# Performance work log

Measured on AMD Instinct MI355X. Metric: run time of the kernel, lower is better.

## Reference

```python
import jax, jax.numpy as jnp
import numpy as np

D_MODEL = 1024
D_INNER = 2048   # expand * d_model
D_STATE = 128
NGROUPS = 1
HEADDIM = 64
NHEADS = D_INNER // HEADDIM  # 32
D_CONV = 4
CHUNK = 256
EPS = 1e-5


def setup_inputs() -> dict:
    key = jax.random.key(0)
    ks = jax.random.split(key, 6)
    B, L = 2, 2048
    d_in_proj = 2 * D_INNER + 2 * NGROUPS * D_STATE + NHEADS  # 4384
    conv_dim = D_INNER + 2 * NGROUPS * D_STATE                # 2304
    u = jax.random.normal(ks[0], (B, L, D_MODEL), jnp.float32)
    W_in = jax.random.normal(ks[1], (d_in_proj, D_MODEL), jnp.float32) * 0.02
    conv_w = jax.random.normal(ks[2], (conv_dim, D_CONV), jnp.float32) * 0.2
    conv_b = jnp.zeros((conv_dim,), jnp.float32)
    # dt_bias = inverse-softplus of dt ~ LogUniform(1e-3, 1e-1), as in __init__
    dt = jnp.exp(jax.random.uniform(ks[3], (NHEADS,), jnp.float32)
                 * (np.log(0.1) - np.log(0.001)) + np.log(0.001))
    dt_bias = dt + jnp.log(-jnp.expm1(-dt))
    A_log = jnp.log(jax.random.uniform(ks[4], (NHEADS,), jnp.float32,
                                       minval=1.0, maxval=16.0))
    D_param = jnp.ones((NHEADS,), jnp.float32)
    norm_w = jnp.ones((D_INNER,), jnp.float32)
    return dict(u=u, W_in=W_in, conv_w=conv_w, conv_b=conv_b,
                dt_bias=dt_bias, A_log=A_log, D_param=D_param, norm_w=norm_w)


def _segsum(x):
    # x: (..., T) -> (..., T, T); entry [i, s] = sum_{j in (s, i]} x_j, -inf above diag
    T = x.shape[-1]
    csum = jnp.cumsum(x, -1)
    diff = csum[..., :, None] - csum[..., None, :]
    mask = jnp.tril(jnp.ones((T, T), dtype=bool))
    return jnp.where(mask, diff, -jnp.inf)


def reference(u, W_in, conv_w, conv_b, dt_bias, A_log, D_param, norm_w):
    B, L, _ = u.shape
    zxbcdt = u @ W_in.T  # (B, L, 2*d_inner + 2*g*N + H)
    z, xBC, dt = jnp.split(zxbcdt, [D_INNER, 2 * D_INNER + 2 * NGROUPS * D_STATE], axis=-1)

    # fused causal depthwise conv1d + silu
    xp = jnp.pad(xBC, ((0, 0), (D_CONV - 1, 0), (0, 0)))
    xc = conv_b
    for k in range(D_CONV):
        xc = xc + xp[:, k:k + L, :] * conv_w[:, k]
    xBC = jax.nn.silu(xc)

    x, Bm, Cm = jnp.split(xBC, [D_INNER, D_INNER + NGROUPS * D_STATE], axis=-1)
    dt = jax.nn.softplus(dt + dt_bias)          # (B, L, H)
    A = -jnp.exp(A_log)                          # (H,)

    x = x.reshape(B, L, NHEADS, HEADDIM)
    Bh = jnp.repeat(Bm.reshape(B, L, NGROUPS, D_STATE), NHEADS // NGROUPS, axis=2)
    Ch = jnp.repeat(Cm.reshape(B, L, NGROUPS, D_STATE), NHEADS // NGROUPS, axis=2)

    # chunked SSD (Mamba2) scan
    nc = L // CHUNK
    xc_ = x.reshape(B, nc, CHUNK, NHEADS, HEADDIM)
    dtc = dt.reshape(B, nc, CHUNK, NHEADS)
    Bc = Bh.reshape(B, nc, CHUNK, NHEADS, D_STATE)
    Cc = Ch.reshape(B, nc, CHUNK, NHEADS, D_STATE)

    a = jnp.moveaxis(dtc * A, -1, 2)             # (B, nc, H, cs)
    a_cum = jnp.cumsum(a, -1)
    Lmat = jnp.exp(_segsum(a))                   # (B, nc, H, cs, cs), lower-tri decay
    xdt = xc_ * dtc[..., None]                   # (B, nc, cs, H, P)

    # intra-chunk (diagonal blocks)
    Y_diag = jnp.einsum('bclhn,bcshn,bchls,bcshp->bclhp', Cc, Bc, Lmat, xdt)

    # chunk-final states and inter-chunk recurrence
    decay_states = jnp.exp(a_cum[..., -1:] - a_cum)         # (B, nc, H, cs)
    states = jnp.einsum('bclhn,bchl,bclhp->bchpn', Bc, decay_states, xdt)
    chunk_decay = jnp.exp(a_cum[..., -1])                   # (B, nc, H)

    def scan_fn(carry, inp):
        s, d = inp                                           # (B,H,P,N), (B,H)
        return carry * d[..., None, None] + s, carry

    init = jnp.zeros((B, NHEADS, HEADDIM, D_STATE), xdt.dtype)
    _, prev_states = jax.lax.scan(scan_fn, init,
                                  (jnp.moveaxis(states, 1, 0),
                                   jnp.moveaxis(chunk_decay, 1, 0)))
    prev_states = jnp.moveaxis(prev_states, 0, 1)            # (B, nc, H, P, N)

    Y_off = jnp.einsum('bclhn,bchpn,bchl->bclhp', Cc, prev_states, jnp.exp(a_cum))

    Y = (Y_diag + Y_off).reshape(B, L, NHEADS, HEADDIM) + D_param[None, None, :, None] * x
    y = Y.reshape(B, L, D_INNER)

    # gated RMSNorm (norm_before_gate=False: gate first, then normalize)
    g = y * jax.nn.silu(z)
    g = g * jax.lax.rsqrt(jnp.mean(g * g, axis=-1, keepdims=True) + EPS) * norm_w
    return g
```

## Files before the change

### kernel.cpp

```cpp
#include <hip/hip_runtime.h>
#include <cstdint>
#include <cmath>

#define KDIM    1024
#define DPROJ   4384
#define NPAD    4480
#define CONVDIM 2304
#define SEQ     2048
#define BATCH   2
#define MROWS   4096
#define NHEADS  32
#define HEADDIM 64
#define DSTATE  128
#define CHUNK   256
#define NCHUNK  8
#define DINNER  2048
#define EPS     1e-5f

typedef unsigned short u16;
typedef float  f32x4  __attribute__((ext_vector_type(4)));
typedef __bf16 bf16x8 __attribute__((ext_vector_type(8)));
typedef u16    u16x8  __attribute__((ext_vector_type(8)));

__device__ __forceinline__ u16 f2bf(float f){
  unsigned u = __builtin_bit_cast(unsigned, f);
  u += 0x7fffu + ((u >> 16) & 1u);
  return (u16)(u >> 16);
}
__device__ __forceinline__ float bf2f(u16 s){
  unsigned u = ((unsigned)s) << 16;
  return __builtin_bit_cast(float, u);
}
__device__ __forceinline__ void gl_lds16(const void* g, void* l){
  __builtin_amdgcn_global_load_lds((const __attribute__((address_space(1))) void*)g,
                                   (__attribute__((address_space(3))) void*)l, 16, 0, 0);
}
__device__ __forceinline__ float sigmoidf_(float x){ return 1.f / (1.f + expf(-x)); }

__global__ __launch_bounds__(256) void k_cvt(const float* __restrict__ u_in, u16* __restrict__ u_out,
                                             const float* __restrict__ w_in, u16* __restrict__ w_out){
  int bid = blockIdx.x;
  const float* in; u16* out; size_t i; int wpath = 0;
  if(bid < 4096){ in = u_in; out = u_out; i = ((size_t)bid * 256 + threadIdx.x) * 4; }
  else          { in = w_in; out = w_out; i = ((size_t)(bid - 4096) * 256 + threadIdx.x) * 4; wpath = 1; }
  float4 v = make_float4(0.f,0.f,0.f,0.f);
  if(!wpath || (int)(i >> 10) < DPROJ) v = *(const float4*)(in + i);
  unsigned a = (unsigned)f2bf(v.x) | ((unsigned)f2bf(v.y) << 16);
  unsigned b = (unsigned)f2bf(v.z) | ((unsigned)f2bf(v.w) << 16);
  uint2 o; o.x = a; o.y = b;
  *(uint2*)(out + i) = o;
}

__global__ __launch_bounds__(256) void k_gemm(const u16* __restrict__ A, const u16* __restrict__ B,
                                              u16* __restrict__ zq, float* __restrict__ dtraw){
  __shared__ u16 As[128*32];
  __shared__ u16 Bs[128*32];
  int tid = threadIdx.x;
  int gid = blockIdx.x;
  int mG  = gid / (35*8);
  int rem = gid % (35*8);
  int nblk = rem / 8;
  int mblk = mG*8 + (rem & 7);
  int m0 = mblk * 128, n0 = nblk * 128;
  int w = tid >> 6, lane = tid & 63, r = lane & 15, q = lane >> 4;
  int wm = (w >> 1) * 64, wn = (w & 1) * 64;
  f32x4 acc[4][4] = {};
  const u16* Ag0 = A + (size_t)(m0 +       (tid >> 2)) * KDIM + (tid & 3) * 8;
  const u16* Ag1 = A + (size_t)(m0 + 64 +  (tid >> 2)) * KDIM + (tid & 3) * 8;
  const u16* Bg0 = B + (size_t)(n0 +       (tid >> 2)) * KDIM + (tid & 3) * 8;
  const u16* Bg1 = B + (size_t)(n0 + 64 +  (tid >> 2)) * KDIM + (tid & 3) * 8;
  for(int kt = 0; kt < KDIM/32; kt++){
    int k0 = kt * 32;
    gl_lds16(Ag0 + k0, &As[(size_t)tid * 8]);
    gl_lds16(Ag1 + k0, &As[((size_t)tid + 256) * 8]);
    gl_lds16(Bg0 + k0, &Bs[(size_t)tid * 8]);
    gl_lds16(Bg1 + k0, &Bs[((size_t)tid + 256) * 8]);
    __syncthreads();
    bf16x8 af[4], bfm[4];
    #pragma unroll
    for(int i = 0; i < 4; i++) af[i]  = *(const bf16x8*)&As[(wm + i*16 + r) * 32 + q*8];
    #pragma unroll
    for(int j = 0; j < 4; j++) bfm[j] = *(const bf16x8*)&Bs[(wn + j*16 + r) * 32 + q*8];
    #pragma unroll
    for(int i = 0; i < 4; i++)
      #pragma unroll
      for(int j = 0; j < 4; j++)
        acc[i][j] = __builtin_amdgcn_mfma_f32_16x16x32_bf16(af[i], bfm[j], acc[i][j], 0, 0, 0);
    __syncthreads();
  }
  #pragma unroll
  for(int i = 0; i < 4; i++)
    #pragma unroll
    for(int j = 0; j < 4; j++)
      #pragma unroll
      for(int e = 0; e < 4; e++){
        int row = m0 + wm + i*16 + q*4 + e;
        int col = n0 + wn + j*16 + r;
        zq[(size_t)row * NPAD + col] = f2bf(acc[i][j][e]);
        if(nblk == 34) dtraw[(size_t)row * 128 + (col - 4352)] = acc[i][j][e];
      }
}

__global__ __launch_bounds__(256) void k_conv(const u16* __restrict__ zq,
                                              const float* __restrict__ cw,
                                              const float* __restrict__ cb,
                                              u16* __restrict__ xq, u16* __restrict__ xqT,
                                              u16* __restrict__ Bq, u16* __restrict__ Cq){
  int c0 = blockIdx.x * 64;
  int l0 = blockIdx.y * 64;
  int b  = blockIdx.z;
  int lane = threadIdx.x & 63;
  int c = c0 + lane;
  int lb = l0 + (threadIdx.x >> 6) * 16;
  float wt0 = cw[c*4+0], wt1 = cw[c*4+1], wt2 = cw[c*4+2], wt3 = cw[c*4+3];
  float bias = cb[c];
  const u16* zrow = zq + (size_t)(b*SEQ) * NPAD + 2048 + c;
  float w0 = (lb-3 >= 0) ? bf2f(zrow[(size_t)(lb-3)*NPAD]) : 0.f;
  float w1 = (lb-2 >= 0) ? bf2f(zrow[(size_t)(lb-2)*NPAD]) : 0.f;
  float w2 = (lb-1 >= 0) ? bf2f(zrow[(size_t)(lb-1)*NPAD]) : 0.f;
  u16 vals[16];
  #pragma unroll
  for(int rr = 0; rr < 16; rr++){
    float in3 = bf2f(zrow[(size_t)(lb+rr)*NPAD]);
    float a = bias + w0*wt0 + w1*wt1 + w2*wt2 + in3*wt3;
    vals[rr] = f2bf(a * sigmoidf_(a));
    w0 = w1; w1 = w2; w2 = in3;
  }
  if(blockIdx.x < 32){
    #pragma unroll
    for(int rr = 0; rr < 16; rr++)
      xq[(size_t)(b*SEQ + lb + rr) * DINNER + c] = vals[rr];
    int h = c0 >> 6;
    u16* dst = xqT + ((size_t)((b*32 + h)*64) + lane) * SEQ + lb;
    u16x8 v0, v1;
    #pragma unroll
    for(int m = 0; m < 8; m++){ v0[m] = vals[m]; v1[m] = vals[8+m]; }
    *(u16x8*)dst = v0;
    *(u16x8*)(dst + 8) = v1;
  } else {
    u16* dst; int col;
    if(blockIdx.x < 34){ dst = Bq; col = c0 - 2048 + lane; }
    else               { dst = Cq; col = c0 - 2176 + lane; }
    #pragma unroll
    for(int rr = 0; rr < 16; rr++)
      dst[(size_t)(b*SEQ + lb + rr) * 128 + col] = vals[rr];
  }
}

__global__ __launch_bounds__(256) void k_acum(const float* __restrict__ dtraw,
                                              const float* __restrict__ dt_bias,
                                              const float* __restrict__ A_log,
                                              float* __restrict__ dtb,
                                              float* __restrict__ acum,
                                              float* __restrict__ cdec){
  int bid = blockIdx.x;
  int h = bid & 31, c = (bid >> 5) & 7, b = bid >> 8;
  int t = threadIdx.x;
  __shared__ float sb[256];
  size_t row = (size_t)(b*SEQ + c*CHUNK + t);
  float v = dtraw[row * 128 + h] + dt_bias[h];
  float dt = (v > 20.f) ? v : log1pf(expf(v));
  dtb[row * 32 + h] = dt;
  float Ah = -expf(A_log[h]);
  float a = dt * Ah;
  sb[t] = a; __syncthreads();
  for(int off = 1; off < 256; off <<= 1){
    float vv = (t >= off) ? sb[t - off] : 0.f;
    __syncthreads();
    sb[t] += vv;
    __syncthreads();
  }
  float ac = sb[t];
  acum[(size_t)bid * 256 + t] = ac;
  if(t == 255) cdec[bid] = expf(ac);
}

__global__ __launch_bounds__(256) void k_states(const u16* __restrict__ xqT, const u16* __restrict__ Bq,
                                                const float* __restrict__ dtb,
                                                const float* __restrict__ acum,
                                                float* __restrict__ states){
  int bid = blockIdx.x;
  int h = bid & 31, c = (bid >> 5) & 7, b = bid >> 8;
  int tid = threadIdx.x;
  int w = tid >> 6, lane = tid & 63, r = lane & 15, q = lane >> 4;
  __shared__ u16 bT[128*72];
  size_t rowB = (size_t)(b*SEQ + c*CHUNK);
  const u16* xrow = xqT + (size_t)((b*32 + h)*64) * SEQ + c*CHUNK;
  float alast = acum[(size_t)bid * 256 + 255];
  f32x4 acc[4][2] = {};
  for(int slab = 0; slab < 4; slab++){
    int lb = slab * 64;
    int l = lane;
    float f = expf(alast - acum[(size_t)bid * 256 + lb + l]) * dtb[(rowB + lb + l) * 32 + h];
    __syncthreads();
    const u16* bp = Bq + (rowB + lb + l) * 128 + w*32;
    #pragma unroll
    for(int k = 0; k < 4; k++){
      u16x8 v = *(const u16x8*)(bp + k*8);
      #pragma unroll
      for(int m = 0; m < 8; m++)
        bT[(w*32 + k*8 + m)*72 + l] = f2bf(bf2f(v[m]) * f);
    }
    __syncthreads();
    #pragma unroll
    for(int ks = 0; ks < 2; ks++){
      bf16x8 af[4], bfr[2];
      #pragma unroll
      for(int i = 0; i < 4; i++)
        af[i] = *(const bf16x8*)&xrow[(size_t)(i*16 + r) * SEQ + lb + ks*32 + q*8];
      #pragma unroll
      for(int j = 0; j < 2; j++) bfr[j] = *(const bf16x8*)&bT[(w*32 + j*16 + r)*72 + ks*32 + q*8];
      #pragma unroll
      for(int i = 0; i < 4; i++)
        #pragma unroll
        for(int j = 0; j < 2; j++)
          acc[i][j] = __builtin_amdgcn_mfma_f32_16x16x32_bf16(af[i], bfr[j], acc[i][j], 0, 0, 0);
    }
  }
  #pragma unroll
  for(int i = 0; i < 4; i++)
    #pragma unroll
    for(int j = 0; j < 2; j++)
      #pragma unroll
      for(int e = 0; e < 4; e++){
        int p = i*16 + q*4 + e;
        int n = w*32 + j*16 + r;
        states[((size_t)bid * 64 + p) * 128 + n] = acc[i][j][e];
      }
}

__global__ __launch_bounds__(256) void k_scan(const float* __restrict__ states,
                                              const float* __restrict__ cdec,
                                              u16* __restrict__ prevb){
  size_t i = (size_t)blockIdx.x * 256 + threadIdx.x;
  int n = (int)(i & 127), p = (int)((i >> 7) & 63), h = (int)((i >> 13) & 31), b = (int)(i >> 18);
  float carry = 0.f;
  for(int c = 0; c < NCHUNK; c++){
    int bch = (b*8 + c)*32 + h;
    size_t off = ((size_t)bch * 64 + p) * 128 + n;
    float s = states[off];
    prevb[off] = f2bf(carry);
    carry = carry * cdec[bch] + s;
  }
}

__global__ __launch_bounds__(128) void k_y(const u16* __restrict__ xqT, const u16* __restrict__ Bq,
                                           const u16* __restrict__ Cq, const float* __restrict__ dtb,
                                           const float* __restrict__ acum, const u16* __restrict__ prevb,
                                           u16* __restrict__ yq){
  int bid = blockIdx.x;
  int bch = bid >> 1, pr = bid & 1;
  int h = bch & 31, c = (bch >> 5) & 7, b = bch >> 8;
  int tid = threadIdx.x;
  int w2 = tid >> 6, lane = tid & 63, r = lane & 15, q = lane >> 4;
  int lt = pr ? (1 + w2) : (w2 * 3);
  int l0 = lt * 64;
  __shared__ float acl[256];
  __shared__ float dts[256];
  __shared__ u16 G[2][64*72];
  size_t rowC = (size_t)(b*SEQ + c*CHUNK);
  #pragma unroll
  for(int it = 0; it < 2; it++){
    int s = it*128 + tid;
    acl[s] = acum[(size_t)bch * 256 + s];
    dts[s] = dtb[(rowC + s) * 32 + h];
  }
  __syncthreads();
  bf16x8 cf[4][4];
  #pragma unroll
  for(int i = 0; i < 4; i++)
    #pragma unroll
    for(int ks = 0; ks < 4; ks++)
      cf[i][ks] = *(const bf16x8*)&Cq[(rowC + l0 + i*16 + r) * 128 + ks*32 + q*8];
  f32x4 accY[4][4] = {};
  #pragma unroll
  for(int ks = 0; ks < 4; ks++){
    #pragma unroll
    for(int j = 0; j < 4; j++){
      bf16x8 bfr = *(const bf16x8*)&prevb[((size_t)bch * 64 + j*16 + r) * 128 + ks*32 + q*8];
      #pragma unroll
      for(int i = 0; i < 4; i++)
        accY[i][j] = __builtin_amdgcn_mfma_f32_16x16x32_bf16(cf[i][ks], bfr, accY[i][j], 0, 0, 0);
    }
  }
  #pragma unroll
  for(int i = 0; i < 4; i++)
    #pragma unroll
    for(int e = 0; e < 4; e++){
      float sc = expf(acl[l0 + i*16 + q*4 + e]);
      #pragma unroll
      for(int j = 0; j < 4; j++) accY[i][j][e] *= sc;
    }
  const u16* xrow = xqT + (size_t)((b*32 + h)*64) * SEQ + c*CHUNK;
  u16* Gw = G[w2];
  for(int st = 0; st <= lt; st++){
    int s0 = st * 64;
    f32x4 accS[4][4] = {};
    #pragma unroll
    for(int ks = 0; ks < 4; ks++){
      #pragma unroll
      for(int j = 0; j < 4; j++){
        bf16x8 bfr = *(const bf16x8*)&Bq[(rowC + s0 + j*16 + r) * 128 + ks*32 + q*8];
        #pragma unroll
        for(int i = 0; i < 4; i++)
          accS[i][j] = __builtin_amdgcn_mfma_f32_16x16x32_bf16(cf[i][ks], bfr, accS[i][j], 0, 0, 0);
      }
    }
    #pragma unroll
    for(int i = 0; i < 4; i++)
      #pragma unroll
      for(int j = 0; j < 4; j++)
        #pragma unroll
        for(int e = 0; e < 4; e++){
          int ll = l0 + i*16 + q*4 + e;
          int ss = s0 + j*16 + r;
          float v = (ll >= ss) ? accS[i][j][e] * expf(acl[ll] - acl[ss]) * dts[ss] : 0.f;
          Gw[(i*16 + q*4 + e)*72 + j*16 + r] = f2bf(v);
        }
    #pragma unroll
    for(int ks = 0; ks < 2; ks++){
      bf16x8 gf[4], xf[4];
      #pragma unroll
      for(int i = 0; i < 4; i++) gf[i] = *(const bf16x8*)&Gw[(i*16 + r)*72 + ks*32 + q*8];
      #pragma unroll
      for(int j = 0; j < 4; j++)
        xf[j] = *(const bf16x8*)&xrow[(size_t)(j*16 + r) * SEQ + s0 + ks*32 + q*8];
      #pragma unroll
      for(int i = 0; i < 4; i++)
        #pragma unroll
        for(int j = 0; j < 4; j++)
          accY[i][j] = __builtin_amdgcn_mfma_f32_16x16x32_bf16(gf[i], xf[j], accY[i][j], 0, 0, 0);
    }
  }
  #pragma unroll
  for(int i = 0; i < 4; i++)
    #pragma unroll
    for(int j = 0; j < 4; j++)
      #pragma unroll
      for(int e = 0; e < 4; e++){
        int ll = l0 + i*16 + q*4 + e;
        int p = j*16 + r;
        yq[(rowC + ll) * (size_t)DINNER + h*64 + p] = f2bf(accY[i][j][e]);
      }
}

__global__ __launch_bounds__(256) void k_norm(const u16* __restrict__ yq, const u16* __restrict__ xq,
                                              const u16* __restrict__ zq, const float* __restrict__ Dp,
                                              const float* __restrict__ nw, float* __restrict__ out){
  int bl = blockIdx.x;
  int t = threadIdx.x;
  float Dh = Dp[t >> 3];
  u16x8 yv = *(const u16x8*)(yq + (size_t)bl * DINNER + t*8);
  u16x8 xv = *(const u16x8*)(xq + (size_t)bl * DINNER + t*8);
  u16x8 zv = *(const u16x8*)(zq + (size_t)bl * NPAD + t*8);
  float g[8];
  float ss = 0.f;
  #pragma unroll
  for(int m = 0; m < 8; m++){
    float y = bf2f(yv[m]) + Dh * bf2f(xv[m]);
    float z = bf2f(zv[m]);
    float v = y * (z * sigmoidf_(z));
    g[m] = v;
    ss += v * v;
  }
  #pragma unroll
  for(int off = 32; off > 0; off >>= 1) ss += __shfl_down(ss, off, 64);
  __shared__ float wsum[4];
  if((t & 63) == 0) wsum[t >> 6] = ss;
  __syncthreads();
  float tot = wsum[0] + wsum[1] + wsum[2] + wsum[3];
  float scale = rsqrtf(tot / (float)DINNER + EPS);
  float4 o0, o1;
  o0.x = g[0]*scale*nw[t*8+0]; o0.y = g[1]*scale*nw[t*8+1];
  o0.z = g[2]*scale*nw[t*8+2]; o0.w = g[3]*scale*nw[t*8+3];
  o1.x = g[4]*scale*nw[t*8+4]; o1.y = g[5]*scale*nw[t*8+5];
  o1.z = g[6]*scale*nw[t*8+6]; o1.w = g[7]*scale*nw[t*8+7];
  *(float4*)(out + (size_t)bl * DINNER + t*8)     = o0;
  *(float4*)(out + (size_t)bl * DINNER + t*8 + 4) = o1;
}

extern "C" void kernel_launch(void* const* d_in, const int* in_sizes, int n_in,
                              void* d_out, int out_size, void* d_ws, size_t ws_size,
                              hipStream_t stream){
  const float* u    = (const float*)d_in[0];
  const float* W    = (const float*)d_in[1];
  const float* cw   = (const float*)d_in[2];
  const float* cb   = (const float*)d_in[3];
  const float* dtbi = (const float*)d_in[4];
  const float* Alog = (const float*)d_in[5];
  const float* Dp   = (const float*)d_in[6];
  const float* nw   = (const float*)d_in[7];
  float* out = (float*)d_out;

  char* ws = (char*)d_ws;
  size_t off = 0;
  auto alloc = [&](size_t bytes) -> void* {
    void* p = ws + off;
    off += (bytes + 255) & ~(size_t)255;
    return p;
  };
  u16*   u_bf    = (u16*)  alloc((size_t)MROWS * KDIM * 2);
  u16*   W_bf    = (u16*)  alloc((size_t)NPAD * KDIM * 2);
  u16*   zq      = (u16*)  alloc((size_t)MROWS * NPAD * 2);
  float* dtraw   = (float*)alloc((size_t)MROWS * 128 * 4);
  u16*   xq      = (u16*)  alloc((size_t)MROWS * DINNER * 2);
  u16*   xqT     = (u16*)  alloc((size_t)MROWS * DINNER * 2);
  u16*   Bq      = (u16*)  alloc((size_t)MROWS * 128 * 2);
  u16*   Cq      = (u16*)  alloc((size_t)MROWS * 128 * 2);
  float* dtb     = (float*)alloc((size_t)MROWS * 32 * 4);
  float* acum    = (float*)alloc((size_t)512 * 256 * 4);
  float* cdec    = (float*)alloc((size_t)512 * 4);
  float* states  = (float*)alloc((size_t)512 * 64 * 128 * 4);
  u16*   prevb   = (u16*)  alloc((size_t)512 * 64 * 128 * 2);
  u16*   yq      = (u16*)  alloc((size_t)MROWS * DINNER * 2);

  k_cvt<<<4096 + 4480, 256, 0, stream>>>(u, u_bf, W, W_bf);
  k_gemm<<<35*32, 256, 0, stream>>>(u_bf, W_bf, zq, dtraw);
  k_conv<<<dim3(36, 32, 2), 256, 0, stream>>>(zq, cw, cb, xq, xqT, Bq, Cq);
  k_acum<<<512, 256, 0, stream>>>(dtraw, dtbi, Alog, dtb, acum, cdec);
  k_states<<<512, 256, 0, stream>>>(xqT, Bq, dtb, acum, states);
  k_scan<<<((size_t)BATCH*NHEADS*64*128)/256, 256, 0, stream>>>(states, cdec, prevb);
  k_y<<<1024, 128, 0, stream>>>(xqT, Bq, Cq, dtb, acum, prevb, yq);
  k_norm<<<MROWS, 256, 0, stream>>>(yq, xq, zq, Dp, nw, out);
}
```

Baseline: 305.3 us.

## Deepen GEMM K-tile, vectorize conv over four channels, store states in bf16

The input-projection GEMM now stages 64-wide K tiles in LDS instead of 32, halving the number of barrier-separated iterations and issuing more MFMAs per sync. The conv kernel has each thread handle four adjacent channels, using 8-byte vector loads and stores and a quarter as many blocks. The chunk states buffer is stored as bf16 rather than fp32, halving the traffic between the states and scan kernels at some cost in precision of the inter-chunk recurrence input.

Result: no change. 304.1 us (-0.4%).

```diff
diff --git a/kernel.cpp b/kernel.cpp
--- a/kernel.cpp
+++ b/kernel.cpp
@@ -21,6 +21,7 @@
 typedef float  f32x4  __attribute__((ext_vector_type(4)));
 typedef __bf16 bf16x8 __attribute__((ext_vector_type(8)));
 typedef u16    u16x8  __attribute__((ext_vector_type(8)));
+typedef u16    u16x4  __attribute__((ext_vector_type(4)));
 
 __device__ __forceinline__ u16 f2bf(float f){
   unsigned u = __builtin_bit_cast(unsigned, f);
@@ -53,8 +54,8 @@
 
 __global__ __launch_bounds__(256) void k_gemm(const u16* __restrict__ A, const u16* __restrict__ B,
                                               u16* __restrict__ zq, float* __restrict__ dtraw){
-  __shared__ u16 As[128*32];
-  __shared__ u16 Bs[128*32];
+  __shared__ u16 As[128*64];
+  __shared__ u16 Bs[128*64];
   int tid = threadIdx.x;
   int gid = blockIdx.x;
   int mG  = gid / (35*8);
@@ -65,27 +66,29 @@
   int w = tid >> 6, lane = tid & 63, r = lane & 15, q = lane >> 4;
   int wm = (w >> 1) * 64, wn = (w & 1) * 64;
   f32x4 acc[4][4] = {};
-  const u16* Ag0 = A + (size_t)(m0 +       (tid >> 2)) * KDIM + (tid & 3) * 8;
-  const u16* Ag1 = A + (size_t)(m0 + 64 +  (tid >> 2)) * KDIM + (tid & 3) * 8;
-  const u16* Bg0 = B + (size_t)(n0 +       (tid >> 2)) * KDIM + (tid & 3) * 8;
-  const u16* Bg1 = B + (size_t)(n0 + 64 +  (tid >> 2)) * KDIM + (tid & 3) * 8;
-  for(int kt = 0; kt < KDIM/32; kt++){
-    int k0 = kt * 32;
-    gl_lds16(Ag0 + k0, &As[(size_t)tid * 8]);
-    gl_lds16(Ag1 + k0, &As[((size_t)tid + 256) * 8]);
-    gl_lds16(Bg0 + k0, &Bs[(size_t)tid * 8]);
-    gl_lds16(Bg1 + k0, &Bs[((size_t)tid + 256) * 8]);
-    __syncthreads();
-    bf16x8 af[4], bfm[4];
-    #pragma unroll
-    for(int i = 0; i < 4; i++) af[i]  = *(const bf16x8*)&As[(wm + i*16 + r) * 32 + q*8];
-    #pragma unroll
-    for(int j = 0; j < 4; j++) bfm[j] = *(const bf16x8*)&Bs[(wn + j*16 + r) * 32 + q*8];
-    #pragma unroll
-    for(int i = 0; i < 4; i++)
-      #pragma unroll
-      for(int j = 0; j < 4; j++)
-        acc[i][j] = __builtin_amdgcn_mfma_f32_16x16x32_bf16(af[i], bfm[j], acc[i][j], 0, 0, 0);
+  const u16* Ag = A + (size_t)(m0 + (tid >> 3)) * KDIM + (tid & 7) * 8;
+  const u16* Bg = B + (size_t)(n0 + (tid >> 3)) * KDIM + (tid & 7) * 8;
+  for(int kt = 0; kt < KDIM/64; kt++){
+    int k0 = kt * 64;
+    #pragma unroll
+    for(int m = 0; m < 4; m++){
+      gl_lds16(Ag + (size_t)m*32*KDIM + k0, &As[((size_t)m*256 + tid) * 8]);
+      gl_lds16(Bg + (size_t)m*32*KDIM + k0, &Bs[((size_t)m*256 + tid) * 8]);
+    }
+    __syncthreads();
+    #pragma unroll
+    for(int ks = 0; ks < 2; ks++){
+      bf16x8 af[4], bfm[4];
+      #pragma unroll
+      for(int i = 0; i < 4; i++) af[i]  = *(const bf16x8*)&As[(wm + i*16 + r) * 64 + ks*32 + q*8];
+      #pragma unroll
+      for(int j = 0; j < 4; j++) bfm[j] = *(const bf16x8*)&Bs[(wn + j*16 + r) * 64 + ks*32 + q*8];
+      #pragma unroll
+      for(int i = 0; i < 4; i++)
+        #pragma unroll
+        for(int j = 0; j < 4; j++)
+          acc[i][j] = __builtin_amdgcn_mfma_f32_16x16x32_bf16(af[i], bfm[j], acc[i][j], 0, 0, 0);
+    }
     __syncthreads();
   }
   #pragma unroll
@@ -106,44 +109,68 @@
                                               const float* __restrict__ cb,
                                               u16* __restrict__ xq, u16* __restrict__ xqT,
                                               u16* __restrict__ Bq, u16* __restrict__ Cq){
-  int c0 = blockIdx.x * 64;
+  int c0 = blockIdx.x * 256;
   int l0 = blockIdx.y * 64;
   int b  = blockIdx.z;
-  int lane = threadIdx.x & 63;
-  int c = c0 + lane;
-  int lb = l0 + (threadIdx.x >> 6) * 16;
-  float wt0 = cw[c*4+0], wt1 = cw[c*4+1], wt2 = cw[c*4+2], wt3 = cw[c*4+3];
-  float bias = cb[c];
-  const u16* zrow = zq + (size_t)(b*SEQ) * NPAD + 2048 + c;
-  float w0 = (lb-3 >= 0) ? bf2f(zrow[(size_t)(lb-3)*NPAD]) : 0.f;
-  float w1 = (lb-2 >= 0) ? bf2f(zrow[(size_t)(lb-2)*NPAD]) : 0.f;
-  float w2 = (lb-1 >= 0) ? bf2f(zrow[(size_t)(lb-1)*NPAD]) : 0.f;
-  u16 vals[16];
+  int tid = threadIdx.x;
+  int cbase = c0 + (tid & 63) * 4;
+  int lb = l0 + (tid >> 6) * 16;
+  float wt[4][4], bias[4];
+  #pragma unroll
+  for(int cc = 0; cc < 4; cc++){
+    float4 wv = *(const float4*)(cw + (cbase + cc)*4);
+    wt[cc][0]=wv.x; wt[cc][1]=wv.y; wt[cc][2]=wv.z; wt[cc][3]=wv.w;
+    bias[cc] = cb[cbase + cc];
+  }
+  const u16* zrow = zq + (size_t)(b*SEQ) * NPAD + 2048 + cbase;
+  float w0[4] = {}, w1[4] = {}, w2[4] = {};
+  if(lb-3 >= 0){ u16x4 v = *(const u16x4*)(zrow + (size_t)(lb-3)*NPAD);
+    #pragma unroll
+    for(int cc=0;cc<4;cc++) w0[cc] = bf2f(v[cc]); }
+  if(lb-2 >= 0){ u16x4 v = *(const u16x4*)(zrow + (size_t)(lb-2)*NPAD);
+    #pragma unroll
+    for(int cc=0;cc<4;cc++) w1[cc] = bf2f(v[cc]); }
+  if(lb-1 >= 0){ u16x4 v = *(const u16x4*)(zrow + (size_t)(lb-1)*NPAD);
+    #pragma unroll
+    for(int cc=0;cc<4;cc++) w2[cc] = bf2f(v[cc]); }
+  u16 vals[16][4];
   #pragma unroll
   for(int rr = 0; rr < 16; rr++){
-    float in3 = bf2f(zrow[(size_t)(lb+rr)*NPAD]);
-    float a = bias + w0*wt0 + w1*wt1 + w2*wt2 + in3*wt3;
-    vals[rr] = f2bf(a * sigmoidf_(a));
-    w0 = w1; w1 = w2; w2 = in3;
-  }
-  if(blockIdx.x < 32){
-    #pragma unroll
-    for(int rr = 0; rr < 16; rr++)
-      xq[(size_t)(b*SEQ + lb + rr) * DINNER + c] = vals[rr];
-    int h = c0 >> 6;
-    u16* dst = xqT + ((size_t)((b*32 + h)*64) + lane) * SEQ + lb;
-    u16x8 v0, v1;
-    #pragma unroll
-    for(int m = 0; m < 8; m++){ v0[m] = vals[m]; v1[m] = vals[8+m]; }
-    *(u16x8*)dst = v0;
-    *(u16x8*)(dst + 8) = v1;
+    u16x4 v = *(const u16x4*)(zrow + (size_t)(lb+rr)*NPAD);
+    #pragma unroll
+    for(int cc = 0; cc < 4; cc++){
+      float in3 = bf2f(v[cc]);
+      float a = bias[cc] + w0[cc]*wt[cc][0] + w1[cc]*wt[cc][1] + w2[cc]*wt[cc][2] + in3*wt[cc][3];
+      vals[rr][cc] = f2bf(a * sigmoidf_(a));
+      w0[cc] = w1[cc]; w1[cc] = w2[cc]; w2[cc] = in3;
+    }
+  }
+  if(blockIdx.x < 8){
+    #pragma unroll
+    for(int rr = 0; rr < 16; rr++){
+      u16x4 o; o[0]=vals[rr][0]; o[1]=vals[rr][1]; o[2]=vals[rr][2]; o[3]=vals[rr][3];
+      *(u16x4*)(xq + (size_t)(b*SEQ + lb + rr) * DINNER + cbase) = o;
+    }
+    #pragma unroll
+    for(int cc = 0; cc < 4; cc++){
+      int c = cbase + cc;
+      int h = c >> 6, p = c & 63;
+      u16* dst = xqT + ((size_t)((b*32 + h)*64) + p) * SEQ + lb;
+      u16x8 v0, v1;
+      #pragma unroll
+      for(int m = 0; m < 8; m++){ v0[m] = vals[m][cc]; v1[m] = vals[8+m][cc]; }
+      *(u16x8*)dst = v0;
+      *(u16x8*)(dst + 8) = v1;
+    }
   } else {
-    u16* dst; int col;
-    if(blockIdx.x < 34){ dst = Bq; col = c0 - 2048 + lane; }
-    else               { dst = Cq; col = c0 - 2176 + lane; }
-    #pragma unroll
-    for(int rr = 0; rr < 16; rr++)
-      dst[(size_t)(b*SEQ + lb + rr) * 128 + col] = vals[rr];
+    int col = cbase - 2048;
+    u16* dst = (col < 128) ? Bq : Cq;
+    int c4 = col & 127;
+    #pragma unroll
+    for(int rr = 0; rr < 16; rr++){
+      u16x4 o; o[0]=vals[rr][0]; o[1]=vals[rr][1]; o[2]=vals[rr][2]; o[3]=vals[rr][3];
+      *(u16x4*)(dst + (size_t)(b*SEQ + lb + rr) * 128 + c4) = o;
+    }
   }
 }
 
@@ -178,7 +205,7 @@
 __global__ __launch_bounds__(256) void k_states(const u16* __restrict__ xqT, const u16* __restrict__ Bq,
                                                 const float* __restrict__ dtb,
                                                 const float* __restrict__ acum,
-                                                float* __restrict__ states){
+                                                u16* __restrict__ states){
   int bid = blockIdx.x;
   int h = bid & 31, c = (bid >> 5) & 7, b = bid >> 8;
   int tid = threadIdx.x;
@@ -225,11 +252,11 @@
       for(int e = 0; e < 4; e++){
         int p = i*16 + q*4 + e;
         int n = w*32 + j*16 + r;
-        states[((size_t)bid * 64 + p) * 128 + n] = acc[i][j][e];
+        states[((size_t)bid * 64 + p) * 128 + n] = f2bf(acc[i][j][e]);
       }
 }
 
-__global__ __launch_bounds__(256) void k_scan(const float* __restrict__ states,
+__global__ __launch_bounds__(256) void k_scan(const u16* __restrict__ states,
                                               const float* __restrict__ cdec,
                                               u16* __restrict__ prevb){
   size_t i = (size_t)blockIdx.x * 256 + threadIdx.x;
@@ -238,7 +265,7 @@
   for(int c = 0; c < NCHUNK; c++){
     int bch = (b*8 + c)*32 + h;
     size_t off = ((size_t)bch * 64 + p) * 128 + n;
-    float s = states[off];
+    float s = bf2f(states[off]);
     prevb[off] = f2bf(carry);
     carry = carry * cdec[bch] + s;
   }
@@ -410,13 +437,13 @@
   float* dtb     = (float*)alloc((size_t)MROWS * 32 * 4);
   float* acum    = (float*)alloc((size_t)512 * 256 * 4);
   float* cdec    = (float*)alloc((size_t)512 * 4);
-  float* states  = (float*)alloc((size_t)512 * 64 * 128 * 4);
+  u16*   states  = (u16*)  alloc((size_t)512 * 64 * 128 * 2);
   u16*   prevb   = (u16*)  alloc((size_t)512 * 64 * 128 * 2);
   u16*   yq      = (u16*)  alloc((size_t)MROWS * DINNER * 2);
 
   k_cvt<<<4096 + 4480, 256, 0, stream>>>(u, u_bf, W, W_bf);
   k_gemm<<<35*32, 256, 0, stream>>>(u_bf, W_bf, zq, dtraw);
-  k_conv<<<dim3(36, 32, 2), 256, 0, stream>>>(zq, cw, cb, xq, xqT, Bq, Cq);
+  k_conv<<<dim3(9, 32, 2), 256, 0, stream>>>(zq, cw, cb, xq, xqT, Bq, Cq);
   k_acum<<<512, 256, 0, stream>>>(dtraw, dtbi, Alog, dtb, acum, cdec);
   k_states<<<512, 256, 0, stream>>>(xqT, Bq, dtb, acum, states);
   k_scan<<<((size_t)BATCH*NHEADS*64*128)/256, 256, 0, stream>>>(states, cdec, prevb);
```
